# Kernel optimization log

Hardware: AMD Instinct MI355X
Metric: run time of the kernel (lower is better)

The kernel has to match this reference:

```python
import jax, jax.numpy as jnp
import numpy as np

B, N, PD = 4, 4096, 1024
D, S = 16, 64              # max_span, span_dim
ALL = D * S                # 1024

# fwd[t, tau] = tau - t if 0 <= tau - t < D else D (points at padding slot)
FWD = np.array([[tau - t if 0 <= tau - t < D else D for tau in range(2 * D)]
                for t in range(D)], dtype=np.int32)           # [D, 2D]
BWD = np.array([[t + d for d in range(D)] for t in range(D)], dtype=np.int32)  # [D, D]
T_IDX = np.arange(D, dtype=np.int32)


def _gather(x, idx, padding):
    # x: [B, N, D, S]; pad span dim, reshape seq into blocks of D, gather spans.
    # out[b, n, t, j, s] = x_padded[b, n, t, idx[t, j], s]  -> [B, N//D, D, idx.shape[1], S]
    b, n, d, s = x.shape
    pad = jnp.full((b, n, 1, s), padding, dtype=x.dtype)
    x = jnp.concatenate([x, pad], axis=2).reshape(b, n // d, d, d + 1, s)
    return x[:, :, T_IDX[:, None], idx, :]


def setup_inputs() -> dict:
    key = jax.random.key(0)
    k1, k2, k3, k4, k5 = jax.random.split(key, 5)
    return {
        "x":   jax.random.normal(k1, (B, N, PD), jnp.float32),
        "W_r": jax.random.normal(k2, (PD, 2 * ALL), jnp.float32) * 0.02,
        "b_r": jax.random.normal(k3, (2 * ALL,), jnp.float32) * 0.02,
        "W_w": jax.random.normal(k4, (ALL, PD), jnp.float32) * 0.02,
        "b_w": jax.random.normal(k5, (PD,), jnp.float32) * 0.02,
    }


def reference(x, W_r, b_r, W_w, b_w):
    # reader: Linear(PD -> 2*ALL), split into left/right span logits
    P = (x @ W_r + b_r).reshape(B, N, 2, D, S)
    L = P[:, :, 0]                                  # [B, N, D, S]
    R = jnp.roll(P[:, :, 1], -1, axis=1)            # roll(-1) along seq
    Lg = _gather(L, FWD, -10000.0)                  # [B, T, D, 2D, S]
    Rg = _gather(R, np.roll(FWD, 1, axis=1), 0.0)   # [B, T, D, 2D, S]
    Lg = jnp.transpose(Lg, (0, 1, 4, 2, 3))         # [B, T, S, D, 2D]
    Rg = jnp.transpose(Rg, (0, 1, 4, 2, 3))
    Lg = jax.nn.softmax(Lg, axis=-1)
    L0, L1 = Lg[..., :D], Lg[..., D:]
    R0, R1 = Rg[..., :D], Rg[..., D:]
    Q0 = L0 @ R0                                    # [B, T, S, D, D]
    Q1 = L0 @ R1 + L1 @ jnp.roll(R0, -1, axis=1)
    mask = jnp.ones((Q1.shape[1],), Q1.dtype).at[-1].set(0.0)  # zero last block
    Q1 = Q1 * mask[None, :, None, None, None]
    Q = jnp.concatenate([Q0, Q1], axis=-1)          # [B, T, S, D, 2D]
    Q = jnp.transpose(Q, (0, 1, 3, 4, 2))           # [B, T, D, 2D, S]
    Q = Q[:, :, T_IDX[:, None], BWD, :]             # [B, T, D, D, S]
    out = Q.reshape(B, N, ALL)
    return out @ W_w + b_w                          # writer: Linear(ALL -> PD)
```

## Files before the change

### kernel.cpp

```cpp
#include <hip/hip_runtime.h>
#include <hip/hip_bf16.h>

#define B_ 4
#define N_ 4096
#define PD_ 1024
#define D_ 16
#define S_ 64
#define ALL_ 1024
#define TWOALL_ 2048
#define M_ 16384

typedef __bf16 bf16x8 __attribute__((ext_vector_type(8)));
typedef float floatx4 __attribute__((ext_vector_type(4)));

__device__ __forceinline__ float bf2f(unsigned short u) {
    union { unsigned int i; float f; } v;
    v.i = ((unsigned int)u) << 16;
    return v.f;
}

__device__ __forceinline__ unsigned short f2bf(float f) {
    unsigned int x = __float_as_uint(f);
    unsigned int r = (x + 0x7fffu + ((x >> 16) & 1u)) >> 16;
    return (unsigned short)r;
}

__device__ __forceinline__ void load_lds_16(const void* g, void* l) {
    __builtin_amdgcn_global_load_lds(
        (const __attribute__((address_space(1))) void*)g,
        (__attribute__((address_space(3))) void*)l, 16, 0, 0);
}

__global__ __launch_bounds__(256) void convert_f32_bf16(
    const float* __restrict__ in, unsigned short* __restrict__ out, int n4) {
    int i = blockIdx.x * 256 + threadIdx.x;
    if (i >= n4) return;
    float4 v = *(const float4*)(in + (size_t)i * 4);
    ushort4 o;
    o.x = f2bf(v.x); o.y = f2bf(v.y); o.z = f2bf(v.z); o.w = f2bf(v.w);
    *(ushort4*)(out + (size_t)i * 4) = o;
}

__global__ void transpose_f32_bf16(const float* __restrict__ in,
                                   unsigned short* __restrict__ out,
                                   int rows, int cols) {
    __shared__ float tile[32][33];
    int bx = blockIdx.x * 32;
    int by = blockIdx.y * 32;
    int tx = threadIdx.x;
    int ty = threadIdx.y;
    #pragma unroll
    for (int i = 0; i < 32; i += 8)
        tile[ty + i][tx] = in[(size_t)(by + ty + i) * cols + bx + tx];
    __syncthreads();
    #pragma unroll
    for (int i = 0; i < 32; i += 8)
        out[(size_t)(bx + ty + i) * rows + by + tx] = f2bf(tile[tx][ty + i]);
}

#define BM 256
#define BN 256
#define BK 64

#define STAGE_A(buf_, h_, kt_) do { \
    load_lds_16(a_base + (size_t)((h_) * 128) * K + (kt_) * 64, \
                &As[buf_][((h_) * 128 + wave * 16) * 64]); \
    load_lds_16(a_base + (size_t)((h_) * 128 + 8) * K + (kt_) * 64, \
                &As[buf_][((h_) * 128 + wave * 16 + 8) * 64]); \
  } while (0)

#define STAGE_B(buf_, h_, kt_) do { \
    load_lds_16(b_base + (size_t)((h_) * 128) * K + (kt_) * 64, \
                &Bs[buf_][((h_) * 128 + wave * 16) * 64]); \
    load_lds_16(b_base + (size_t)((h_) * 128 + 8) * K + (kt_) * 64, \
                &Bs[buf_][((h_) * 128 + wave * 16 + 8) * 64]); \
  } while (0)

#define LOAD_BF(n_) do { \
    const unsigned short* p_ = Bb + (wn * 64 + (n_) * 16 + lrow) * 64; \
    bfr[n_][0] = *(const bf16x8*)(p_ + ((g0 ^ (lrow & 7)) * 8)); \
    bfr[n_][1] = *(const bf16x8*)(p_ + (((g0 + 4) ^ (lrow & 7)) * 8)); \
  } while (0)

#define MMA16(n_) do { \
    __builtin_amdgcn_s_setprio(1); \
    _Pragma("unroll") \
    for (int kk = 0; kk < 2; ++kk) { \
      _Pragma("unroll") \
      for (int m = 0; m < 8; ++m) \
        acc[m][n_] = __builtin_amdgcn_mfma_f32_16x16x32_bf16( \
            af[m][kk], bfr[n_][kk], acc[m][n_], 0, 0, 0); \
    } \
    __builtin_amdgcn_s_setprio(0); \
  } while (0)

#define POST_BAR() do { \
    __builtin_amdgcn_s_barrier(); \
    __builtin_amdgcn_sched_barrier(0); \
  } while (0)

template <int OUT_BF>
__global__ __launch_bounds__(512, 2) void gemm_bf16(
    const unsigned short* __restrict__ A,
    const unsigned short* __restrict__ Bt,
    const float* __restrict__ bias,
    void* __restrict__ Cv,
    int M, int N, int K, int gxl, int gypx) {

    __shared__ __align__(16) unsigned short As[2][BM * BK];
    __shared__ __align__(16) unsigned short Bs[2][BN * BK];

    const int tid  = threadIdx.x;
    const int lane = tid & 63;
    const int wave = tid >> 6;
    const int wm   = wave & 1;
    const int wn   = wave >> 1;

    const int flat = blockIdx.x;
    const int xcd  = flat & 7;
    const int slot = flat >> 3;
    const int bx   = slot & ((1 << gxl) - 1);
    const int by   = xcd * gypx + (slot >> gxl);
    const int bm0  = by * BM;
    const int bn0  = bx * BN;

    const int lrow = lane & 15;
    const int g0   = lane >> 4;

    const int srow = lane >> 3;
    const int sg   = (lane & 7) ^ srow;

    const unsigned short* a_base =
        A + (size_t)(bm0 + wave * 16 + srow) * K + sg * 8;
    const unsigned short* b_base =
        Bt + (size_t)(bn0 + wave * 16 + srow) * K + sg * 8;

    floatx4 acc[8][4] = {};
    bf16x8 af[8][2], bfr[4][2];

    const int NTk = K >> 6;

    STAGE_A(0, 0, 0); STAGE_A(0, 1, 0); STAGE_B(0, 0, 0); STAGE_B(0, 1, 0);
    if (NTk > 1) {
        STAGE_A(1, 0, 1); STAGE_A(1, 1, 1); STAGE_B(1, 0, 1);
        asm volatile("s_waitcnt vmcnt(6)" ::: "memory");
    } else {
        asm volatile("s_waitcnt vmcnt(0)" ::: "memory");
    }
    POST_BAR();

    for (int t = 0; t < NTk; ++t) {
        const int buf = t & 1;
        const unsigned short* Ab = As[buf];
        const unsigned short* Bb = Bs[buf];

        #pragma unroll
        for (int m = 0; m < 8; ++m) {
            const unsigned short* p_ = Ab + (wm * 128 + m * 16 + lrow) * 64;
            af[m][0] = *(const bf16x8*)(p_ + ((g0 ^ (lrow & 7)) * 8));
            af[m][1] = *(const bf16x8*)(p_ + (((g0 + 4) ^ (lrow & 7)) * 8));
        }
        LOAD_BF(0);
        if (t + 1 < NTk) STAGE_B((t + 1) & 1, 1, t + 1);
        __builtin_amdgcn_s_barrier();
        asm volatile("s_waitcnt lgkmcnt(0)" ::: "memory");
        MMA16(0);
        POST_BAR();

        LOAD_BF(1);
        LOAD_BF(2);
        if (t + 2 < NTk) STAGE_A(buf, 0, t + 2);
        __builtin_amdgcn_s_barrier();
        asm volatile("s_waitcnt lgkmcnt(0)" ::: "memory");
        MMA16(1);
        POST_BAR();

        LOAD_BF(3);
        if (t + 2 < NTk) STAGE_A(buf, 1, t + 2);
        __builtin_amdgcn_s_barrier();
        asm volatile("s_waitcnt lgkmcnt(0)" ::: "memory");
        MMA16(2);
        POST_BAR();

        if (t + 2 < NTk) STAGE_B(buf, 0, t + 2);
        __builtin_amdgcn_s_barrier();
        MMA16(3);
        if (t + 2 < NTk) {
            asm volatile("s_waitcnt vmcnt(6)" ::: "memory");
        } else if (t + 1 < NTk) {
            asm volatile("s_waitcnt vmcnt(0)" ::: "memory");
        }
        POST_BAR();
    }

    #pragma unroll
    for (int n = 0; n < 4; ++n) {
        int col = bn0 + wn * 64 + n * 16 + (lane & 15);
        float bv = bias[col];
        #pragma unroll
        for (int m = 0; m < 8; ++m) {
            #pragma unroll
            for (int r = 0; r < 4; ++r) {
                int row = bm0 + wm * 128 + m * 16 + (lane >> 4) * 4 + r;
                float v = acc[m][n][r] + bv;
                if (OUT_BF)
                    ((unsigned short*)Cv)[(size_t)row * N + col] = f2bf(v);
                else
                    ((float*)Cv)[(size_t)row * N + col] = v;
            }
        }
    }
}

__global__ __launch_bounds__(256) void middle_kernel(
    const unsigned short* __restrict__ P,
    unsigned short* __restrict__ A2) {

    int idx = blockIdx.x * 256 + threadIdx.x;
    int s   = idx & 63;
    int r   = idx >> 6;
    int n   = r & (N_ - 1);
    const int t = n & (D_ - 1);
    const int c = n >> 4;

    const unsigned short* Lp = P + (size_t)r * TWOALL_ + s;
    float w[16];
    float mx = -1e30f;
    #pragma unroll
    for (int j = 0; j < 16; ++j) {
        w[j] = bf2f(Lp[j * S_]);
        mx = fmaxf(mx, w[j]);
    }
    float sum = 0.f;
    #pragma unroll
    for (int j = 0; j < 16; ++j) {
        w[j] = __expf(w[j] - mx);
        sum += w[j];
    }
    float inv = 1.0f / sum;

    float q[16];
    #pragma unroll
    for (int d = 0; d < 16; ++d) q[d] = 0.f;

    #pragma unroll
    for (int i = 0; i < 15; ++i) {
        int np = n + i + 1;
        if (np >= N_) np -= N_;
        int b = r >> 12;
        const unsigned short* Rp = P + (((size_t)(b * N_ + np)) * 2 + 1) * ALL_ + s;
        #pragma unroll
        for (int k = 0; k < 15 - i; ++k) {
            q[i + k + 1] += w[i] * bf2f(Rp[k * S_]);
        }
    }

    unsigned short* out = A2 + (size_t)r * ALL_ + s;
    bool last = (c == (N_ / D_) - 1);
    #pragma unroll
    for (int d = 0; d < 16; ++d) {
        float v = (d == 0) ? 0.f : q[d] * inv;
        if (last && (t + d >= D_)) v = 0.f;
        out[d * S_] = f2bf(v);
    }
}

extern "C" void kernel_launch(void* const* d_in, const int* in_sizes, int n_in,
                              void* d_out, int out_size, void* d_ws, size_t ws_size,
                              hipStream_t stream) {
    const float* x   = (const float*)d_in[0];
    const float* W_r = (const float*)d_in[1];
    const float* b_r = (const float*)d_in[2];
    const float* W_w = (const float*)d_in[3];
    const float* b_w = (const float*)d_in[4];
    float* out = (float*)d_out;

    unsigned short* ws  = (unsigned short*)d_ws;
    unsigned short* P   = ws;
    unsigned short* xbf = P   + (size_t)M_ * TWOALL_;
    unsigned short* A2  = xbf + (size_t)M_ * ALL_;
    unsigned short* WrT = A2  + (size_t)M_ * ALL_;
    unsigned short* WwT = WrT + (size_t)TWOALL_ * PD_;

    convert_f32_bf16<<<dim3((M_ * PD_ / 4 + 255) / 256), 256, 0, stream>>>(
        x, xbf, M_ * PD_ / 4);

    dim3 tb(32, 8);
    transpose_f32_bf16<<<dim3(TWOALL_ / 32, PD_ / 32), tb, 0, stream>>>(W_r, WrT, PD_, TWOALL_);
    transpose_f32_bf16<<<dim3(ALL_ / 32, PD_ / 32), tb, 0, stream>>>(W_w, WwT, PD_, ALL_);

    gemm_bf16<1><<<dim3((TWOALL_ / BN) * (M_ / BM)), 512, 0, stream>>>(
        xbf, WrT, b_r, P, M_, TWOALL_, PD_, 3, (M_ / BM) / 8);

    middle_kernel<<<dim3((B_ * N_ * S_) / 256), 256, 0, stream>>>(P, A2);

    gemm_bf16<0><<<dim3((ALL_ / BN) * (M_ / BM)), 512, 0, stream>>>(
        A2, WwT, b_w, out, M_, ALL_, PD_, 2, (M_ / BM) / 8);
}
```

Before: 289.3 us.

## Restructure GEMM inner loop into quadrant MMAs to halve A-fragment registers

The per-k-tile inner loop now runs as four 4x2 MFMA quadrants instead of four 8x1 column passes. Only half of the A fragments (4 rows) are held at a time, and B is split into two half-fragments that are reused across the A halves. This lowers VGPR pressure and changes the order of LDS reads and global-to-LDS staging relative to the barriers. The A tile is now re-read from LDS for the second half, and the reworked waitcnt and barrier sequence adds some synchronisation risk.

Result: no change. 293.1 us (+1.3%).

```diff
diff --git a/kernel.cpp b/kernel.cpp
--- a/kernel.cpp
+++ b/kernel.cpp
@@ -76,22 +76,40 @@
                 &Bs[buf_][((h_) * 128 + wave * 16 + 8) * 64]); \
   } while (0)
 
-#define LOAD_BF(n_) do { \
-    const unsigned short* p_ = Bb + (wn * 64 + (n_) * 16 + lrow) * 64; \
-    bfr[n_][0] = *(const bf16x8*)(p_ + ((g0 ^ (lrow & 7)) * 8)); \
-    bfr[n_][1] = *(const bf16x8*)(p_ + (((g0 + 4) ^ (lrow & 7)) * 8)); \
-  } while (0)
-
-#define MMA16(n_) do { \
+#define LOAD_AF(mh_) do { \
+    _Pragma("unroll") \
+    for (int i = 0; i < 4; ++i) { \
+        const unsigned short* p_ = Ab + (wm * 128 + (mh_) * 64 + i * 16 + lrow) * 64; \
+        af[i][0] = *(const bf16x8*)(p_ + ((g0 ^ (lrow & 7)) * 8)); \
+        af[i][1] = *(const bf16x8*)(p_ + (((g0 + 4) ^ (lrow & 7)) * 8)); \
+    } } while (0)
+
+#define LOAD_BH(dst_, nh_) do { \
+    _Pragma("unroll") \
+    for (int j = 0; j < 2; ++j) { \
+        const unsigned short* p_ = Bb + (wn * 64 + (nh_) * 32 + j * 16 + lrow) * 64; \
+        dst_[j][0] = *(const bf16x8*)(p_ + ((g0 ^ (lrow & 7)) * 8)); \
+        dst_[j][1] = *(const bf16x8*)(p_ + (((g0 + 4) ^ (lrow & 7)) * 8)); \
+    } } while (0)
+
+#define MMA_Q(mh_, nh_, bq_) do { \
     __builtin_amdgcn_s_setprio(1); \
     _Pragma("unroll") \
-    for (int kk = 0; kk < 2; ++kk) { \
+    for (int kk = 0; kk < 2; ++kk) \
       _Pragma("unroll") \
-      for (int m = 0; m < 8; ++m) \
-        acc[m][n_] = __builtin_amdgcn_mfma_f32_16x16x32_bf16( \
-            af[m][kk], bfr[n_][kk], acc[m][n_], 0, 0, 0); \
-    } \
+      for (int i = 0; i < 4; ++i) \
+        _Pragma("unroll") \
+        for (int j = 0; j < 2; ++j) \
+          acc[(mh_) * 4 + i][(nh_) * 2 + j] = \
+              __builtin_amdgcn_mfma_f32_16x16x32_bf16( \
+                  af[i][kk], bq_[j][kk], acc[(mh_) * 4 + i][(nh_) * 2 + j], 0, 0, 0); \
     __builtin_amdgcn_s_setprio(0); \
+  } while (0)
+
+#define MID_BAR() do { \
+    __builtin_amdgcn_sched_barrier(0); \
+    __builtin_amdgcn_s_barrier(); \
+    asm volatile("s_waitcnt lgkmcnt(0)" ::: "memory"); \
   } while (0)
 
 #define POST_BAR() do { \
@@ -136,7 +154,9 @@
         Bt + (size_t)(bn0 + wave * 16 + srow) * K + sg * 8;
 
     floatx4 acc[8][4] = {};
-    bf16x8 af[8][2], bfr[4][2];
+    bf16x8 af[4][2];
+    bf16x8 bf0[2][2];
+    bf16x8 bf1[2][2];
 
     const int NTk = K >> 6;
 
@@ -154,37 +174,29 @@
         const unsigned short* Ab = As[buf];
         const unsigned short* Bb = Bs[buf];
 
-        #pragma unroll
-        for (int m = 0; m < 8; ++m) {
-            const unsigned short* p_ = Ab + (wm * 128 + m * 16 + lrow) * 64;
-            af[m][0] = *(const bf16x8*)(p_ + ((g0 ^ (lrow & 7)) * 8));
-            af[m][1] = *(const bf16x8*)(p_ + (((g0 + 4) ^ (lrow & 7)) * 8));
-        }
-        LOAD_BF(0);
+        LOAD_AF(0);
+        LOAD_BH(bf0, 0);
         if (t + 1 < NTk) STAGE_B((t + 1) & 1, 1, t + 1);
+        asm volatile("s_waitcnt lgkmcnt(8)" ::: "memory");
+        MID_BAR();
+        MMA_Q(0, 0, bf0);
+        POST_BAR();
+
+        LOAD_BH(bf1, 1);
+        MID_BAR();
+        MMA_Q(0, 1, bf1);
+        POST_BAR();
+
+        LOAD_AF(1);
+        if (t + 2 < NTk) STAGE_B(buf, 0, t + 2);
+        MID_BAR();
+        MMA_Q(1, 1, bf1);
+        POST_BAR();
+
+        if (t + 2 < NTk) { STAGE_A(buf, 0, t + 2); STAGE_A(buf, 1, t + 2); }
+        __builtin_amdgcn_sched_barrier(0);
         __builtin_amdgcn_s_barrier();
-        asm volatile("s_waitcnt lgkmcnt(0)" ::: "memory");
-        MMA16(0);
-        POST_BAR();
-
-        LOAD_BF(1);
-        LOAD_BF(2);
-        if (t + 2 < NTk) STAGE_A(buf, 0, t + 2);
-        __builtin_amdgcn_s_barrier();
-        asm volatile("s_waitcnt lgkmcnt(0)" ::: "memory");
-        MMA16(1);
-        POST_BAR();
-
-        LOAD_BF(3);
-        if (t + 2 < NTk) STAGE_A(buf, 1, t + 2);
-        __builtin_amdgcn_s_barrier();
-        asm volatile("s_waitcnt lgkmcnt(0)" ::: "memory");
-        MMA16(2);
-        POST_BAR();
-
-        if (t + 2 < NTk) STAGE_B(buf, 0, t + 2);
-        __builtin_amdgcn_s_barrier();
-        MMA16(3);
+        MMA_Q(1, 0, bf0);
         if (t + 2 < NTk) {
             asm volatile("s_waitcnt vmcnt(6)" ::: "memory");
         } else if (t + 1 < NTk) {
```
